# Kernel tuning notes

Measured on AMD Instinct MI355X. Metric: run time of the kernel, lower is better.

## Reference

```python
import jax, jax.numpy as jnp
import numpy as np

HID = 2048
NH = 16
NKV = 16
HD = HID // NH          # 128
ROPE_BASE = 100000.0
ROPE_SCALE = 4.0
B, L = 2, 2048
NEG = -1e9


def rope(x, offset=0):
    # x: [B, NH, L, HD]; half-split (rotate-half) RoPE with linear scaling
    Lx = x.shape[2]
    D = HD // 2
    pos = (jnp.arange(offset, offset + Lx, dtype=jnp.float32) / ROPE_SCALE)  # [L]
    freq = jnp.exp(-jnp.arange(D, dtype=jnp.float32) * (np.log(ROPE_BASE) / D))  # [D]
    m_theta = pos[:, None] * freq[None, :]          # [L, D]
    cos, sin = jnp.cos(m_theta), jnp.sin(m_theta)
    x1, x2 = x[..., :D], x[..., D:]
    rx1 = x1 * cos - x2 * sin
    rx2 = x1 * sin + x2 * cos
    return jnp.concatenate([rx1, rx2], axis=-1)


def setup_inputs() -> dict:
    key = jax.random.key(0)
    ks = jax.random.split(key, 5)
    x = jax.random.normal(ks[0], (B, L, HID), dtype=jnp.float32)
    # additive causal mask [1,1,L,L]
    mask = jnp.triu(jnp.full((L, L), NEG, dtype=jnp.float32), k=1)[None, None]
    Wq = jax.random.normal(ks[1], (HID, NH * HD), dtype=jnp.float32) * 0.02
    Wk = jax.random.normal(ks[2], (HID, NKV * HD), dtype=jnp.float32) * 0.02
    Wv = jax.random.normal(ks[3], (HID, NKV * HD), dtype=jnp.float32) * 0.02
    Wo = jax.random.normal(ks[4], (NH * HD, HID), dtype=jnp.float32) * 0.02
    return {"x": x, "mask": mask, "Wq": Wq, "Wk": Wk, "Wv": Wv, "Wo": Wo}


def reference(x, mask, Wq, Wk, Wv, Wo):
    b, l, _ = x.shape
    scale = HD ** -0.5
    q = (x @ Wq).reshape(b, l, NH, HD).transpose(0, 2, 1, 3)    # [B,NH,L,HD]
    k = (x @ Wk).reshape(b, l, NKV, HD).transpose(0, 2, 1, 3)
    v = (x @ Wv).reshape(b, l, NKV, HD).transpose(0, 2, 1, 3)
    rep = NH // NKV
    if rep > 1:
        k = jnp.repeat(k, rep, axis=1)
        v = jnp.repeat(v, rep, axis=1)
    q = rope(q)
    k = rope(k)
    scores = scale * jnp.einsum('bhqd,bhkd->bhqk', q, k)        # [B,NH,L,L]
    scores = scores + mask
    attn = jax.nn.softmax(scores, axis=-1)
    out = jnp.einsum('bhqk,bhkd->bhqd', attn, v)                # [B,NH,L,HD]
    out = out.transpose(0, 2, 1, 3).reshape(b, l, NH * HD)
    return out @ Wo
```

## Files before the change

kernel.cpp:

```cpp
#include <hip/hip_runtime.h>
#include <math.h>

#define BB   2
#define LL   2048
#define HIDD 2048
#define NHH  16
#define HDD  128
#define QKN  4096
#define THR2 11.5416f

typedef unsigned short u16;
typedef float  f32x4 __attribute__((ext_vector_type(4)));
typedef __bf16 bf16x8 __attribute__((ext_vector_type(8)));

static __device__ __forceinline__ float exp2_fast(float x){
  return __builtin_amdgcn_exp2f(x);
}
static __device__ __forceinline__ u16 f2bf(float x){
  unsigned u = __float_as_uint(x);
  return (u16)((u + 0x7fffu + ((u >> 16) & 1u)) >> 16);
}
static __device__ __forceinline__ float bf2f(u16 b){
  return __uint_as_float(((unsigned)b) << 16);
}
static __device__ __forceinline__ void gl_lds16(const void* g, void* l){
  __builtin_amdgcn_global_load_lds(
      (__attribute__((address_space(1))) void*)(void*)g,
      (__attribute__((address_space(3))) void*)l,
      16, 0, 0);
}


__global__ void cvt_f32_bf16_k(const float* __restrict__ src, u16* __restrict__ dst, int n4){
  int i = blockIdx.x * blockDim.x + threadIdx.x;
  if (i >= n4) return;
  float4 v = ((const float4*)src)[i];
  ushort4 o;
  o.x = f2bf(v.x); o.y = f2bf(v.y); o.z = f2bf(v.z); o.w = f2bf(v.w);
  ((ushort4*)dst)[i] = o;
}

__global__ void rope_table_k(float2* __restrict__ tab){
  int idx = blockIdx.x * blockDim.x + threadIdx.x;
  int l = idx >> 6, d = idx & 63;
  float fr = __expf(-(float)d * 0.17988946f);
  float th = (float)l * 0.25f * fr;
  float s, c;
  sincosf(th, &s, &c);
  tab[idx] = make_float2(c, s);
}

__global__ __launch_bounds__(256) void transpose_cvt4_k(
    const float* __restrict__ Wq, const float* __restrict__ Wk,
    const float* __restrict__ Wv, const float* __restrict__ Wo,
    u16* __restrict__ Wt, u16* __restrict__ Wot)
{
  __shared__ u16 t[64][66];
  const int z = blockIdx.z;
  const float* src = (z == 0) ? Wq : (z == 1) ? Wk : (z == 2) ? Wv : Wo;
  u16* dst = (z == 3) ? Wot : (Wt + (size_t)z * 2048 * 2048);
  const int c0 = blockIdx.x * 64, r0 = blockIdx.y * 64;
  const int tid = threadIdx.x;

  #pragma unroll
  for (int i = 0; i < 4; i++){
    int r  = i * 16 + (tid >> 4);
    int c4 = (tid & 15) * 4;
    float4 v = *(const float4*)&src[(size_t)(r0 + r) * 2048 + c0 + c4];
    t[c4 + 0][r] = f2bf(v.x);
    t[c4 + 1][r] = f2bf(v.y);
    t[c4 + 2][r] = f2bf(v.z);
    t[c4 + 3][r] = f2bf(v.w);
  }
  __syncthreads();
  #pragma unroll
  for (int i = 0; i < 2; i++){
    int c  = i * 32 + (tid >> 3);
    int rs = (tid & 7) * 8;
    const unsigned* p = (const unsigned*)&t[c][rs];
    unsigned w0 = p[0], w1 = p[1], w2 = p[2], w3 = p[3];
    u16* d = &dst[(size_t)(c0 + c) * 2048 + r0 + rs];
    ((unsigned*)d)[0] = w0; ((unsigned*)d)[1] = w1;
    ((unsigned*)d)[2] = w2; ((unsigned*)d)[3] = w3;
  }
}


__global__ __launch_bounds__(256) void gemm_qkv_k(
    const u16* __restrict__ A, const u16* __restrict__ Bt,
    u16* __restrict__ qk, u16* __restrict__ vt,
    const float2* __restrict__ rtab, int M, int N, int K)
{
  __shared__ __align__(16) u16 SH[16640];
  u16* As = SH;
  u16* Bs = SH + 8192;
  const int tid = threadIdx.x, lane = tid & 63, wv = tid >> 6;
  const int wr = wv >> 1, wc = wv & 1;
  const int m0 = blockIdx.y * 128, n0 = blockIdx.x * 128;
  const int rq = lane >> 4, cl = lane & 15;

  const f32x4 Z = {0.f, 0.f, 0.f, 0.f};
  f32x4 acc[4][4];
  #pragma unroll
  for (int m = 0; m < 4; m++)
    #pragma unroll
    for (int n = 0; n < 4; n++) acc[m][n] = Z;

  for (int kt = 0; kt < K; kt += 64){
    #pragma unroll
    for (int i = 0; i < 4; i++){
      int fb = (i * 4 + wv) * 64;
      int p  = (fb + lane) * 16;
      int r  = p >> 7;
      int cbs = (p & 127) ^ ((r & 7) << 4);
      gl_lds16(A  + (size_t)(m0 + r) * K + kt + (cbs >> 1), &As[fb * 8]);
      gl_lds16(Bt + (size_t)(n0 + r) * K + kt + (cbs >> 1), &Bs[fb * 8]);
    }
    __syncthreads();
    #pragma unroll
    for (int ks = 0; ks < 2; ks++){
      const int kb = ks * 64 + rq * 16;
      bf16x8 a[4], b[4];
      #pragma unroll
      for (int m = 0; m < 4; m++){
        int r = wr * 64 + m * 16 + cl;
        a[m] = *(const bf16x8*)((const char*)As + r * 128 + (kb ^ ((r & 7) << 4)));
      }
      #pragma unroll
      for (int n = 0; n < 4; n++){
        int r = wc * 64 + n * 16 + cl;
        b[n] = *(const bf16x8*)((const char*)Bs + r * 128 + (kb ^ ((r & 7) << 4)));
      }
      #pragma unroll
      for (int m = 0; m < 4; m++)
        #pragma unroll
        for (int n = 0; n < 4; n++)
          acc[m][n] = __builtin_amdgcn_mfma_f32_16x16x32_bf16(a[m], b[n], acc[m][n], 0, 0, 0);
    }
    __syncthreads();
  }

  const int hd  = n0 >> 7;
  const int sec = hd >> 4;
  const int hh  = hd & 15;

  #pragma unroll
  for (int m = 0; m < 4; m++){
    int gr0 = wr * 64 + m * 16 + rq * 4;
    #pragma unroll
    for (int n = 0; n < 4; n++){
      int gc = wc * 64 + n * 16 + cl;
      #pragma unroll
      for (int rr = 0; rr < 4; rr++)
        SH[(gr0 + rr) * 130 + gc] = f2bf(acc[m][n][rr]);
    }
  }
  __syncthreads();

  if (sec < 2){
    const float fsc = (sec == 0) ? 0.12753375f : 1.0f;
    const int r = tid >> 1, dbase = (tid & 1) * 32;
    const int l = (m0 + r) & (LL - 1);
    const float2* tab = rtab + l * 64 + dbase;
    u16* orow = qk + (size_t)(m0 + r) * QKN + hd * 128;
    #pragma unroll
    for (int g = 0; g < 4; g++){
      bf16x8 o1, o2;
      #pragma unroll
      for (int i = 0; i < 8; i++){
        int d = g * 8 + i;
        float2 cs = tab[d];
        float x1 = bf2f(SH[r * 130 + dbase + d]);
        float x2 = bf2f(SH[r * 130 + dbase + d + 64]);
        o1[i] = (__bf16)((x1 * cs.x - x2 * cs.y) * fsc);
        o2[i] = (__bf16)((x1 * cs.y + x2 * cs.x) * fsc);
      }
      *(bf16x8*)(orow + dbase + g * 8)      = o1;
      *(bf16x8*)(orow + dbase + 64 + g * 8) = o2;
    }
  } else {
    const int d = tid >> 1, l0 = (tid & 1) * 64;
    const int bh = ((m0 >> 11) << 4) + hh;
    u16* vrow = vt + ((size_t)bh * HDD + d) * LL + (m0 & (LL - 1)) + l0;
    #pragma unroll
    for (int g = 0; g < 8; g++){
      bf16x8 o;
      #pragma unroll
      for (int i = 0; i < 8; i++)
        o[i] = *(__bf16*)&SH[(l0 + g * 8 + i) * 130 + d];
      *(bf16x8*)(vrow + g * 8) = o;
    }
  }
}


#define G2_STAGE(kt, bsel) do {                                                           \
  _Pragma("unroll")                                                                       \
  for (int i_ = 0; i_ < 2; i_++){                            \
    int c_ = ((i_ * 8 + wv) * 64) + lane;                                                 \
    int p_ = c_ * 16;                                                                     \
    int r_ = p_ >> 7; int cb_ = (p_ & 127) ^ ((r_ & 7) << 4);                             \
    gl_lds16(A + (size_t)(m0 + r_) * K + (kt) + (cb_ >> 1),                               \
             &AB[bsel][((i_ * 8 + wv) * 64) * 8]);                                        \
  }                                                                                       \
  _Pragma("unroll")                                                                       \
  for (int i_ = 0; i_ < 4; i_++){                            \
    int c_ = ((i_ * 8 + wv) * 64) + lane;                                                 \
    int p_ = c_ * 16;                                                                     \
    int r_ = p_ >> 7; int cb_ = (p_ & 127) ^ ((r_ & 7) << 4);                             \
    gl_lds16(Bt + (size_t)(n0 + r_) * K + (kt) + (cb_ >> 1),                              \
             &AB[bsel][8192 + ((i_ * 8 + wv) * 64) * 8]);                                 \
  }                                                                                       \
} while(0)

template<int OUT_BF16>
__global__ __launch_bounds__(512, 1) void gemm_bt2_k(
    const u16* __restrict__ A, const u16* __restrict__ Bt,
    void* __restrict__ Cout, int M, int N, int K)
{
  __shared__ __align__(16) u16 AB[2][24576];
  const int tid = threadIdx.x, lane = tid & 63, wv = tid >> 6;
  const int wr = wv >> 2, wc = wv & 3;
  const int m0 = blockIdx.y * 128, n0 = blockIdx.x * 256;
  const int rq = lane >> 4, cl = lane & 15;
  const int NT = K >> 6;

  const f32x4 Z = {0.f, 0.f, 0.f, 0.f};
  f32x4 acc[4][4];
  #pragma unroll
  for (int m = 0; m < 4; m++)
    #pragma unroll
    for (int n = 0; n < 4; n++) acc[m][n] = Z;

  G2_STAGE(0, 0);
  G2_STAGE(64, 1);
  asm volatile("s_waitcnt vmcnt(6)");
  __builtin_amdgcn_sched_barrier(0);
  __builtin_amdgcn_s_barrier();

  int cur = 0;
  for (int t = 0; t < NT; t++){
    const char* As_ = (const char*)&AB[cur][0];
    const char* Bs_ = (const char*)&AB[cur][8192];

    #pragma unroll
    for (int ks = 0; ks < 2; ks++){
      const int kb = ks * 64 + rq * 16;
      bf16x8 a[4], b[4];
      #pragma unroll
      for (int m = 0; m < 4; m++){
        int r = wr * 64 + m * 16 + cl;
        a[m] = *(const bf16x8*)(As_ + r * 128 + (kb ^ ((r & 7) << 4)));
      }
      #pragma unroll
      for (int n = 0; n < 4; n++){
        int r = wc * 64 + n * 16 + cl;
        b[n] = *(const bf16x8*)(Bs_ + r * 128 + (kb ^ ((r & 7) << 4)));
      }
      __builtin_amdgcn_s_setprio(1);
      #pragma unroll
      for (int m = 0; m < 4; m++)
        #pragma unroll
        for (int n = 0; n < 4; n++)
          acc[m][n] = __builtin_amdgcn_mfma_f32_16x16x32_bf16(a[m], b[n], acc[m][n], 0, 0, 0);
      __builtin_amdgcn_s_setprio(0);
    }

    __builtin_amdgcn_sched_barrier(0);
    __builtin_amdgcn_s_barrier();

    if (t + 2 < NT){
      G2_STAGE((t + 2) * 64, cur);
      asm volatile("s_waitcnt vmcnt(6)");
    } else {
      asm volatile("s_waitcnt vmcnt(0)");
    }
    __builtin_amdgcn_sched_barrier(0);
    __builtin_amdgcn_s_barrier();
    cur ^= 1;
  }

  #pragma unroll
  for (int m = 0; m < 4; m++){
    int gr0 = m0 + wr * 64 + m * 16 + rq * 4;
    #pragma unroll
    for (int n = 0; n < 4; n++){
      int gc = n0 + wc * 64 + n * 16 + cl;
      #pragma unroll
      for (int rr = 0; rr < 4; rr++){
        if (OUT_BF16) ((u16*)Cout)[(size_t)(gr0 + rr) * N + gc] = f2bf(acc[m][n][rr]);
        else          ((float*)Cout)[(size_t)(gr0 + rr) * N + gc] = acc[m][n][rr];
      }
    }
  }
}


#define STAGE_K(jj, bsel) do {                                                            \
  _Pragma("unroll")                                                                       \
  for (int i_ = 0; i_ < 4; i_++){                                                         \
    int fb_ = (i_ * 4 + wv) * 64;                                                         \
    int p_  = (fb_ + lane) * 16;                                                          \
    int r_ = p_ >> 8; int cb_ = (p_ & 255) ^ ((r_ & 7) << 4);                             \
    gl_lds16(qk + (size_t)(b * LL + (jj) * 64 + r_) * QKN + 2048 + h * HDD + (cb_ >> 1),  \
             &Kb[bsel][fb_ * 8]);                                                         \
  }                                                                                       \
} while(0)

#define STAGE_V(jj) do {                                                                  \
  _Pragma("unroll")                                                                       \
  for (int i_ = 0; i_ < 4; i_++){                                                         \
    int fb_ = (i_ * 4 + wv) * 64;                                                         \
    int p_  = (fb_ + lane) * 16;                                                          \
    int r_ = p_ >> 7; int cb_ = (p_ & 127) ^ ((r_ & 7) << 4);                             \
    gl_lds16(vt + (size_t)(bh * HDD + r_) * LL + (jj) * 64 + (cb_ >> 1), &Vs[fb_ * 8]);   \
  }                                                                                       \
} while(0)

__global__ __launch_bounds__(256, 2) void attn_k(
    const u16* __restrict__ qk, const u16* __restrict__ vt,
    u16* __restrict__ aout)
{
  __shared__ __align__(16) u16 Kb[2][64 * 128];
  __shared__ __align__(16) u16 Vs[128 * 64];
  __shared__ __align__(16) u16 Ps[4][1024];
  const int tid = threadIdx.x, lane = tid & 63, wv = tid >> 6;
  const int bh = blockIdx.x;
  const int pr = blockIdx.y;
  const int b = bh >> 4, h = bh & 15;
  const int rq = lane >> 4, cl = lane & 15;

  bf16x8 ones;
  #pragma unroll
  for (int i = 0; i < 8; i++) ones[i] = (__bf16)1.0f;
  const f32x4 Z = {0.f, 0.f, 0.f, 0.f};

  int cur = 0;
  STAGE_K(0, 0);
  asm volatile("s_waitcnt vmcnt(0)" ::: "memory");
  __builtin_amdgcn_sched_barrier(0);
  __builtin_amdgcn_s_barrier();

  #pragma unroll
  for (int ph = 0; ph < 2; ph++){
    const int qt = ph ? pr : (31 - pr);
    const int nj = qt + 1;

    bf16x8 qf[4];
    {
      const u16* qb = qk + (size_t)(b * LL + qt * 64 + wv * 16 + cl) * QKN + h * HDD + rq * 8;
      #pragma unroll
      for (int ks = 0; ks < 4; ks++) qf[ks] = *(const bf16x8*)(qb + ks * 32);
    }

    f32x4 acco[8], accl;
    float mst[4];
    #pragma unroll
    for (int n = 0; n < 8; n++) acco[n] = Z;
    accl = Z;
    #pragma unroll
    for (int rr = 0; rr < 4; rr++) mst[rr] = -INFINITY;

    for (int j = 0; j < nj; j++){
      const bool sn = (j + 1 < nj) || (ph == 0);
      STAGE_V(j);
      if (j + 1 < nj)      STAGE_K(j + 1, cur ^ 1);
      else if (ph == 0)    STAGE_K(0,     cur ^ 1);
      __builtin_amdgcn_sched_barrier(0);
      if (sn) asm volatile("s_waitcnt vmcnt(8)" ::: "memory");
      else    asm volatile("s_waitcnt vmcnt(4)" ::: "memory");
      __builtin_amdgcn_sched_barrier(0);
      __builtin_amdgcn_s_barrier();
      __builtin_amdgcn_sched_barrier(0);

      f32x4 sv[4];
      {
        const char* KsC = (const char*)&Kb[cur][0];
        #pragma unroll
        for (int ct = 0; ct < 4; ct++) sv[ct] = Z;
        #pragma unroll
        for (int ks = 0; ks < 4; ks++){
          const int kb = ks * 64 + rq * 16;
          #pragma unroll
          for (int ct = 0; ct < 4; ct++){
            int r = ct * 16 + cl;
            bf16x8 bfr = *(const bf16x8*)(KsC + r * 256 + (kb ^ ((r & 7) << 4)));
            sv[ct] = __builtin_amdgcn_mfma_f32_16x16x32_bf16(qf[ks], bfr, sv[ct], 0, 0, 0);
          }
        }
      }

      {
        char* pbase = (char*)&Ps[wv][0];
        const bool msk = (j == qt);

        float p4[4][4], lmx[4];
        #pragma unroll
        for (int rr = 0; rr < 4; rr++) lmx[rr] = -1e30f;
        const int qg = qt * 64 + wv * 16 + rq * 4;
        #pragma unroll
        for (int ct = 0; ct < 4; ct++){
          int col = j * 64 + ct * 16 + cl;
          #pragma unroll
          for (int rr = 0; rr < 4; rr++){
            float v = sv[ct][rr];
            if (msk && col > qg + rr) v = -1e30f;
            p4[ct][rr] = v;
            lmx[rr] = fmaxf(lmx[rr], v);
          }
        }
        float need = -1e30f;
        #pragma unroll
        for (int rr = 0; rr < 4; rr++) need = fmaxf(need, lmx[rr] - mst[rr]);
        if (__any(need > THR2)){
          float mx[4];
          #pragma unroll
          for (int rr = 0; rr < 4; rr++) mx[rr] = lmx[rr];
          #pragma unroll
          for (int off = 1; off < 16; off <<= 1)
            #pragma unroll
            for (int rr = 0; rr < 4; rr++)
              mx[rr] = fmaxf(mx[rr], __shfl_xor(mx[rr], off, 64));
          #pragma unroll
          for (int rr = 0; rr < 4; rr++){
            float mn  = fmaxf(mst[rr], mx[rr]);
            float fsc = exp2_fast(mst[rr] - mn);
            mst[rr] = mn;
            accl[rr] *= fsc;
            #pragma unroll
            for (int n = 0; n < 8; n++) acco[n][rr] *= fsc;
          }
        }
        #pragma unroll
        for (int ct = 0; ct < 4; ct++)
          #pragma unroll
          for (int rr = 0; rr < 4; rr++){
            float e = exp2_fast(p4[ct][rr] - mst[rr]);
            int wr = rq * 4 + rr;
            *(u16*)(pbase + wr * 128 + (((ct * 16 + cl) * 2) ^ ((wr & 7) << 4))) = f2bf(e);
          }
      }

      __builtin_amdgcn_sched_barrier(0);
      if (sn) asm volatile("s_waitcnt vmcnt(4)" ::: "memory");
      else    asm volatile("s_waitcnt vmcnt(0)" ::: "memory");
      __builtin_amdgcn_sched_barrier(0);
      __builtin_amdgcn_s_barrier();
      __builtin_amdgcn_sched_barrier(0);

      {
        const char* VsC = (const char*)Vs;
        char* pbase = (char*)&Ps[wv][0];
        #pragma unroll
        for (int ks = 0; ks < 2; ks++){
          const int kvb = ks * 64 + rq * 16;
          bf16x8 pa = *(const bf16x8*)(pbase + cl * 128 + (kvb ^ ((cl & 7) << 4)));
          accl = __builtin_amdgcn_mfma_f32_16x16x32_bf16(pa, ones, accl, 0, 0, 0);
          #pragma unroll
          for (int n = 0; n < 8; n++){
            int r = n * 16 + cl;
            bf16x8 bfr = *(const bf16x8*)(VsC + r * 128 + (kvb ^ ((r & 7) << 4)));
            acco[n] = __builtin_amdgcn_mfma_f32_16x16x32_bf16(pa, bfr, acco[n], 0, 0, 0);
          }
        }
      }

      __builtin_amdgcn_sched_barrier(0);
      __builtin_amdgcn_s_barrier();
      __builtin_amdgcn_sched_barrier(0);
      cur ^= 1;
    }

    #pragma unroll
    for (int rr = 0; rr < 4; rr++){
      float inv = 1.0f / accl[rr];
      size_t grow = (size_t)(b * LL + qt * 64 + wv * 16 + rq * 4 + rr);
      #pragma unroll
      for (int n = 0; n < 8; n++)
        aout[grow * HIDD + h * HDD + n * 16 + cl] = f2bf(acco[n][rr] * inv);
    }
  }
}


extern "C" void kernel_launch(void* const* d_in, const int* in_sizes, int n_in,
                              void* d_out, int out_size, void* d_ws, size_t ws_size,
                              hipStream_t stream)
{
  const float* x  = (const float*)d_in[0];
  const float* Wq = (const float*)d_in[2];
  const float* Wk = (const float*)d_in[3];
  const float* Wv = (const float*)d_in[4];
  const float* Wo = (const float*)d_in[5];
  float* out = (float*)d_out;

  if (ws_size < 120586240ull) return;

  char* ws = (char*)d_ws;
  u16*    xb   = (u16*)(ws);
  u16*    Wt   = (u16*)(ws + 16777216ull);
  u16*    Wot  = (u16*)(ws + 41943040ull);
  u16*    qk   = (u16*)(ws + 50331648ull);
  u16*    vt   = (u16*)(ws + 83886080ull);
  u16*    aout = (u16*)(ws + 100663296ull);
  float2* rtab = (float2*)(ws + 117440512ull);

  cvt_f32_bf16_k<<<2097152 / 256, 256, 0, stream>>>(x, xb, 2097152);
  rope_table_k<<<131072 / 256, 256, 0, stream>>>(rtab);
  transpose_cvt4_k<<<dim3(32, 32, 4), 256, 0, stream>>>(Wq, Wk, Wv, Wo, Wt, Wot);

  gemm_qkv_k<<<dim3(6144 / 128, 4096 / 128), 256, 0, stream>>>(xb, Wt, qk, vt, rtab, 4096, 6144, 2048);

  attn_k<<<dim3(32, 16), 256, 0, stream>>>(qk, vt, aout);

  gemm_bt2_k<0><<<dim3(2048 / 256, 4096 / 128), 512, 0, stream>>>(aout, Wot, out, 4096, 2048, 2048);
}
```

Baseline: 261.3 us.

## Double-buffer V tiles in attention and vectorize QKV epilogue LDS reads

The attention kernel now double-buffers V alongside K, prefetching the next tile's K and V together. This removes the mid-iteration wait and barrier that previously stalled on the current V load. The QKV GEMM epilogue row stride changes from 130 to 136 so rows are 16-byte aligned, which allows vector bf16x8 LDS reads in the RoPE path. The cost is more LDS per block (an extra 16KB for V), which could limit the two-blocks-per-CU occupancy target. Removing the barrier between P writes and P reads relies on each wave using only its own Ps slice.

```diff
diff --git a/kernel.cpp b/kernel.cpp
--- a/kernel.cpp
+++ b/kernel.cpp
@@ -8,6 +8,7 @@
 #define HDD  128
 #define QKN  4096
 #define THR2 11.5416f
+#define EST  136
 
 typedef unsigned short u16;
 typedef float  f32x4 __attribute__((ext_vector_type(4)));
@@ -91,7 +92,7 @@
     u16* __restrict__ qk, u16* __restrict__ vt,
     const float2* __restrict__ rtab, int M, int N, int K)
 {
-  __shared__ __align__(16) u16 SH[16640];
+  __shared__ __align__(16) u16 SH[17408];
   u16* As = SH;
   u16* Bs = SH + 8192;
   const int tid = threadIdx.x, lane = tid & 63, wv = tid >> 6;
@@ -152,7 +153,7 @@
       int gc = wc * 64 + n * 16 + cl;
       #pragma unroll
       for (int rr = 0; rr < 4; rr++)
-        SH[(gr0 + rr) * 130 + gc] = f2bf(acc[m][n][rr]);
+        SH[(gr0 + rr) * EST + gc] = f2bf(acc[m][n][rr]);
     }
   }
   __syncthreads();
@@ -162,16 +163,17 @@
     const int r = tid >> 1, dbase = (tid & 1) * 32;
     const int l = (m0 + r) & (LL - 1);
     const float2* tab = rtab + l * 64 + dbase;
+    const u16* srow = &SH[r * EST];
     u16* orow = qk + (size_t)(m0 + r) * QKN + hd * 128;
     #pragma unroll
     for (int g = 0; g < 4; g++){
+      bf16x8 x1v = *(const bf16x8*)(srow + dbase + g * 8);
+      bf16x8 x2v = *(const bf16x8*)(srow + dbase + 64 + g * 8);
       bf16x8 o1, o2;
       #pragma unroll
       for (int i = 0; i < 8; i++){
-        int d = g * 8 + i;
-        float2 cs = tab[d];
-        float x1 = bf2f(SH[r * 130 + dbase + d]);
-        float x2 = bf2f(SH[r * 130 + dbase + d + 64]);
+        float2 cs = tab[g * 8 + i];
+        float x1 = (float)x1v[i], x2 = (float)x2v[i];
         o1[i] = (__bf16)((x1 * cs.x - x2 * cs.y) * fsc);
         o2[i] = (__bf16)((x1 * cs.y + x2 * cs.x) * fsc);
       }
@@ -187,7 +189,7 @@
       bf16x8 o;
       #pragma unroll
       for (int i = 0; i < 8; i++)
-        o[i] = *(__bf16*)&SH[(l0 + g * 8 + i) * 130 + d];
+        o[i] = *(__bf16*)&SH[(l0 + g * 8 + i) * EST + d];
       *(bf16x8*)(vrow + g * 8) = o;
     }
   }
@@ -307,13 +309,14 @@
   }                                                                                       \
 } while(0)
 
-#define STAGE_V(jj) do {                                                                  \
+#define STAGE_V(jj, bsel) do {                                                            \
   _Pragma("unroll")                                                                       \
   for (int i_ = 0; i_ < 4; i_++){                                                         \
     int fb_ = (i_ * 4 + wv) * 64;                                                         \
     int p_  = (fb_ + lane) * 16;                                                          \
     int r_ = p_ >> 7; int cb_ = (p_ & 127) ^ ((r_ & 7) << 4);                             \
-    gl_lds16(vt + (size_t)(bh * HDD + r_) * LL + (jj) * 64 + (cb_ >> 1), &Vs[fb_ * 8]);   \
+    gl_lds16(vt + (size_t)(bh * HDD + r_) * LL + (jj) * 64 + (cb_ >> 1),                  \
+             &Vb[bsel][fb_ * 8]);                                                         \
   }                                                                                       \
 } while(0)
 
@@ -322,7 +325,7 @@
     u16* __restrict__ aout)
 {
   __shared__ __align__(16) u16 Kb[2][64 * 128];
-  __shared__ __align__(16) u16 Vs[128 * 64];
+  __shared__ __align__(16) u16 Vb[2][128 * 64];
   __shared__ __align__(16) u16 Ps[4][1024];
   const int tid = threadIdx.x, lane = tid & 63, wv = tid >> 6;
   const int bh = blockIdx.x;
@@ -336,10 +339,8 @@
   const f32x4 Z = {0.f, 0.f, 0.f, 0.f};
 
   int cur = 0;
+  STAGE_V(0, 0);
   STAGE_K(0, 0);
-  asm volatile("s_waitcnt vmcnt(0)" ::: "memory");
-  __builtin_amdgcn_sched_barrier(0);
-  __builtin_amdgcn_s_barrier();
 
   #pragma unroll
   for (int ph = 0; ph < 2; ph++){
@@ -363,12 +364,11 @@
 
     for (int j = 0; j < nj; j++){
       const bool sn = (j + 1 < nj) || (ph == 0);
-      STAGE_V(j);
-      if (j + 1 < nj)      STAGE_K(j + 1, cur ^ 1);
-      else if (ph == 0)    STAGE_K(0,     cur ^ 1);
+      if (j + 1 < nj){      STAGE_V(j + 1, cur ^ 1); STAGE_K(j + 1, cur ^ 1); }
+      else if (ph == 0){    STAGE_V(0,     cur ^ 1); STAGE_K(0,     cur ^ 1); }
       __builtin_amdgcn_sched_barrier(0);
       if (sn) asm volatile("s_waitcnt vmcnt(8)" ::: "memory");
-      else    asm volatile("s_waitcnt vmcnt(4)" ::: "memory");
+      else    asm volatile("s_waitcnt vmcnt(0)" ::: "memory");
       __builtin_amdgcn_sched_barrier(0);
       __builtin_amdgcn_s_barrier();
       __builtin_amdgcn_sched_barrier(0);
@@ -441,15 +441,8 @@
           }
       }
 
-      __builtin_amdgcn_sched_barrier(0);
-      if (sn) asm volatile("s_waitcnt vmcnt(4)" ::: "memory");
-      else    asm volatile("s_waitcnt vmcnt(0)" ::: "memory");
-      __builtin_amdgcn_sched_barrier(0);
-      __builtin_amdgcn_s_barrier();
-      __builtin_amdgcn_sched_barrier(0);
-
       {
-        const char* VsC = (const char*)Vs;
+        const char* VsC = (const char*)&Vb[cur][0];
         char* pbase = (char*)&Ps[wv][0];
         #pragma unroll
         for (int ks = 0; ks < 2; ks++){
```

Measured after the change: 259.5 us. No clear change (-0.7%).
